# Kernel optimization log

Measured on AMD Instinct MI355X. Metric: run time of the kernel, lower is better.

The kernel has to match this reference:

```python
import jax, jax.numpy as jnp
import numpy as np

B, N, K = 4, 2048, 30
H = 128   # num_hidden == num_V_dim
E = 128   # num_E_dim
SCALE = 30.0
EPS = 1e-5


def _ln(x, g, b):
    m = jnp.mean(x, axis=-1, keepdims=True)
    v = jnp.mean(jnp.square(x - m), axis=-1, keepdims=True)
    return (x - m) * jax.lax.rsqrt(v + EPS) * g + b


def _gather_nodes(h_V, E_idx):
    # h_V: [B,N,D], E_idx: [B,N,K] -> [B,N,K,D]
    b, n, k = E_idx.shape
    flat = E_idx.reshape(b, n * k)
    g = jnp.take_along_axis(h_V, flat[:, :, None], axis=1)
    return g.reshape(b, n, k, h_V.shape[-1])


def _gelu(x):
    return jax.nn.gelu(x, approximate=False)  # torch GELU default (erf)


def _lin(x, w, b):
    return jnp.einsum('...i,oi->...o', x, w) + b


def setup_inputs() -> dict:
    key = jax.random.key(0)
    ks = jax.random.split(key, 24)
    s = 0.05
    inp = {
        'h_V': jax.random.normal(ks[0], (B, N, H), jnp.float32),
        'h_E': jax.random.normal(ks[1], (B, N, K, E), jnp.float32),
        'E_idx': jax.random.randint(ks[2], (B, N, K), 0, N, jnp.int32),
        'mask_V': jnp.ones((B, N), jnp.float32),
        'mask_attend': jnp.ones((B, N, K), jnp.float32),
        # node-update MLP W1,W2,W3
        'W1_w': jax.random.normal(ks[3], (H, E + 2 * H), jnp.float32) * s,
        'W1_b': jnp.zeros((H,), jnp.float32),
        'W2_w': jax.random.normal(ks[4], (H, H), jnp.float32) * s,
        'W2_b': jnp.zeros((H,), jnp.float32),
        'W3_w': jax.random.normal(ks[5], (H, H), jnp.float32) * s,
        'W3_b': jnp.zeros((H,), jnp.float32),
        # edge-update MLP W11,W12,W13
        'W11_w': jax.random.normal(ks[6], (H, E + 2 * H), jnp.float32) * s,
        'W11_b': jnp.zeros((H,), jnp.float32),
        'W12_w': jax.random.normal(ks[7], (H, H), jnp.float32) * s,
        'W12_b': jnp.zeros((H,), jnp.float32),
        'W13_w': jax.random.normal(ks[8], (E, H), jnp.float32) * s,
        'W13_b': jnp.zeros((E,), jnp.float32),
        # dense FFN
        'Win_w': jax.random.normal(ks[9], (4 * H, H), jnp.float32) * s,
        'Win_b': jnp.zeros((4 * H,), jnp.float32),
        'Wout_w': jax.random.normal(ks[10], (H, 4 * H), jnp.float32) * s,
        'Wout_b': jnp.zeros((H,), jnp.float32),
        # layer norms
        'g1': jnp.ones((H,), jnp.float32), 'b1': jnp.zeros((H,), jnp.float32),
        'g2': jnp.ones((H,), jnp.float32), 'b2': jnp.zeros((H,), jnp.float32),
        'g3': jnp.ones((E,), jnp.float32), 'b3': jnp.zeros((E,), jnp.float32),
    }
    return inp


def reference(h_V, h_E, E_idx, mask_V, mask_attend,
              W1_w, W1_b, W2_w, W2_b, W3_w, W3_b,
              W11_w, W11_b, W12_w, W12_b, W13_w, W13_b,
              Win_w, Win_b, Wout_w, Wout_b,
              g1, b1, g2, b2, g3, b3):
    # --- node update ---
    nb = _gather_nodes(h_V, E_idx)                               # [B,N,K,H]
    hV_exp = jnp.broadcast_to(h_V[:, :, None, :], nb.shape)
    h_EV = jnp.concatenate([hV_exp, h_E, nb], axis=-1)           # [B,N,K,E+2H]
    m = _lin(_gelu(_lin(_gelu(_lin(h_EV, W1_w, W1_b)), W2_w, W2_b)), W3_w, W3_b)
    m = mask_attend[..., None] * m
    dh = jnp.sum(m, axis=-2) / SCALE
    h_V = _ln(h_V + dh, g1, b1)
    dh = _lin(_gelu(_lin(h_V, Win_w, Win_b)), Wout_w, Wout_b)
    h_V = _ln(h_V + dh, g2, b2)
    h_V = mask_V[..., None] * h_V
    # --- edge update ---
    nb = _gather_nodes(h_V, E_idx)
    hV_exp = jnp.broadcast_to(h_V[:, :, None, :], nb.shape)
    h_EV = jnp.concatenate([hV_exp, h_E, nb], axis=-1)
    m = _lin(_gelu(_lin(_gelu(_lin(h_EV, W11_w, W11_b)), W12_w, W12_b)), W13_w, W13_b)
    h_E = _ln(h_E + m, g3, b3)
    return h_V, h_E
```

## Files before the change

kernel.cpp:

```cpp
#include <hip/hip_runtime.h>
#include <math.h>

#define Kn    30
#define Hn    128
#define NB    2048
#define YS    136

#define OFF_W1    0
#define OFF_W2    49152
#define OFF_W3    65536
#define OFF_W11   81920
#define OFF_W12   131072
#define OFF_W13   147456
#define OFF_WIN   163840
#define OFF_WOUT  229376
#define W_TOTAL   294912
#define WS_ZM     524288
#define WS_SS     1048576
#define WS_SN     2097152

typedef __attribute__((ext_vector_type(8)))  short bh8;
typedef __attribute__((ext_vector_type(4)))  short bh4;
typedef __attribute__((ext_vector_type(16))) float fx16;

__device__ __forceinline__ unsigned short f2bf(float f) {
    unsigned int u = __float_as_uint(f);
    u += 0x7fffu + ((u >> 16) & 1u);
    return (unsigned short)(u >> 16);
}
__device__ __forceinline__ float bf2f(unsigned short h) {
    return __uint_as_float(((unsigned int)h) << 16);
}
__device__ __forceinline__ float gelu_f(float x) {
    float u = 0.7978845608028654f * x * (1.0f + 0.044715f * x * x);
    return x / (1.0f + __expf(-2.0f * u));
}
__device__ __forceinline__ fx16 mfma_bf16(bh8 a, bh8 b, fx16 c) {
    return __builtin_amdgcn_mfma_f32_32x32x16_bf16(a, b, c, 0, 0, 0);
}
__device__ __forceinline__ void st_bf4(unsigned short* dst, float4 v) {
    bh4 t;
    t.x = (short)f2bf(v.x); t.y = (short)f2bf(v.y);
    t.z = (short)f2bf(v.z); t.w = (short)f2bf(v.w);
    *(bh4*)dst = t;
}

template<int KS>
__device__ __forceinline__ void gemm_one(const unsigned short* __restrict__ aBase,
                                         const unsigned short* __restrict__ b0,
                                         fx16& acc0) {
    #pragma unroll
    for (int ks = 0; ks < KS; ks++) {
        bh8 a = *(const bh8*)(aBase + ks * 16);
        acc0 = mfma_bf16(a, *(const bh8*)(b0 + ks * 16), acc0);
    }
}

__device__ __forceinline__ void epi_gelu_sg(const fx16& ac, int col, int rowBase,
                                            float bias, const float* __restrict__ sSelf,
                                            const float* __restrict__ nbrCol,
                                            const int* __restrict__ sIdx,
                                            unsigned short* __restrict__ dst, int lane) {
    int ro = rowBase + 4 * (lane >> 5);
    #pragma unroll
    for (int r = 0; r < 16; r++) {
        int row = ro + (r & 3) + 8 * (r >> 2);
        float st = sSelf[((row >= Kn) ? 128 : 0) + col];
        float pn = nbrCol[(size_t)sIdx[row] * Hn];
        dst[row * YS + col] = f2bf(gelu_f(ac[r] + bias + st + pn));
    }
}
__device__ __forceinline__ void epi_gelu(const fx16& ac, int col, int rowBase,
                                         float bias, unsigned short* __restrict__ dst,
                                         int lane) {
    int ro = rowBase + 4 * (lane >> 5);
    #pragma unroll
    for (int r = 0; r < 16; r++) {
        int row = ro + (r & 3) + 8 * (r >> 2);
        dst[row * YS + col] = f2bf(gelu_f(ac[r] + bias));
    }
}
__device__ __forceinline__ void epi_plain(const fx16& ac, int col, int rowBase,
                                          float bias, unsigned short* __restrict__ dst,
                                          int lane) {
    int ro = rowBase + 4 * (lane >> 5);
    #pragma unroll
    for (int r = 0; r < 16; r++) {
        int row = ro + (r & 3) + 8 * (r >> 2);
        dst[row * YS + col] = f2bf(ac[r] + bias);
    }
}

__global__ __launch_bounds__(256) void prep_weights(
    const float* __restrict__ W1, const float* __restrict__ W2,
    const float* __restrict__ W3, const float* __restrict__ W11,
    const float* __restrict__ W12, const float* __restrict__ W13,
    const float* __restrict__ Win, const float* __restrict__ Wout,
    unsigned short* __restrict__ wsbf) {
    int i = blockIdx.x * 256 + threadIdx.x;
    if (i >= W_TOTAL) return;
    float v;
    if      (i < OFF_W2)   v = W1[i - OFF_W1];
    else if (i < OFF_W3)   v = W2[i - OFF_W2];
    else if (i < OFF_W11)  v = W3[i - OFF_W3];
    else if (i < OFF_W12)  v = W11[i - OFF_W11];
    else if (i < OFF_W13)  v = W12[i - OFF_W12];
    else if (i < OFF_WIN)  v = W13[i - OFF_W13];
    else if (i < OFF_WOUT) v = Win[i - OFF_WIN];
    else                   v = Wout[i - OFF_WOUT];
    wsbf[i] = f2bf(v);
}

__global__ __launch_bounds__(256) void self_gemm(
    const float* __restrict__ hv, const unsigned short* __restrict__ wsbf,
    float* __restrict__ s1s, float* __restrict__ s1n) {
    __shared__ __align__(16) unsigned short sA[32 * YS];
    const int tid = threadIdx.x;
    const int p0 = blockIdx.x * 32;
    const unsigned short* W1bf = wsbf + OFF_W1;
    for (int i = tid; i < 1024; i += 256) {
        int r = i >> 5, c4 = (i & 31) << 2;
        float4 v = *(const float4*)(hv + (size_t)(p0 + r) * Hn + c4);
        st_bf4(sA + r * YS + c4, v);
    }
    __syncthreads();
    const int wid = tid >> 6, lane = tid & 63;
    const int lane31 = lane & 31, lk = (lane >> 5) << 3;
    fx16 accS = {}, accN = {};
    const unsigned short* a   = sA + lane31 * YS + lk;
    const unsigned short* bwS = W1bf + (size_t)(32 * wid + lane31) * 384 + lk;
    const unsigned short* bwN = bwS + 256;
    #pragma unroll
    for (int ks = 0; ks < 8; ks++) {
        bh8 av = *(const bh8*)(a + ks * 16);
        accS = mfma_bf16(av, *(const bh8*)(bwS + ks * 16), accS);
        accN = mfma_bf16(av, *(const bh8*)(bwN + ks * 16), accN);
    }
    int col = 32 * wid + lane31;
    #pragma unroll
    for (int r = 0; r < 16; r++) {
        int row = (r & 3) + 8 * (r >> 2) + 4 * (lane >> 5);
        s1s[(size_t)(p0 + row) * Hn + col] = accS[r];
        s1n[(size_t)(p0 + row) * Hn + col] = accN[r];
    }
}

__global__ __launch_bounds__(512, 8) void node_msg_mfma(
    const float* __restrict__ h_E, const int* __restrict__ E_idx,
    const float* __restrict__ mask_attend,
    const unsigned short* __restrict__ wsbf,
    const float* __restrict__ s1s, const float* __restrict__ s1n,
    const float* __restrict__ W1_b, const float* __restrict__ W2_b,
    unsigned short* __restrict__ zbf, float* __restrict__ zm) {
    __shared__ __align__(16) unsigned short sX[64 * YS];
    __shared__ __align__(16) unsigned short sY[64 * YS];
    __shared__ float sS1[256];
    __shared__ float sMask[64];
    __shared__ int   sIdx[64];

    const int tid = threadIdx.x;
    const int p0 = blockIdx.x * 2;
    const int bB = p0 >> 11;
    const unsigned short* W1bf = wsbf + OFF_W1;
    const unsigned short* W2bf = wsbf + OFF_W2;

    for (int i = tid; i < 1920; i += 512) {
        int r = i >> 5, c4 = (i & 31) << 2;
        float4 v = *(const float4*)(h_E + ((size_t)(p0 * Kn + r)) * Hn + c4);
        st_bf4(sX + r * YS + c4, v);
    }
    if (tid < 272)
        ((unsigned int*)(sX + 60 * YS))[tid] = 0;
    if (tid < 64) {
        int g = tid >> 5, c4 = (tid & 31) << 2;
        *(float4*)(sS1 + g * 128 + c4) = *(const float4*)(s1s + (size_t)(p0 + g) * Hn + c4);
    }
    if (tid < 60) sMask[tid] = mask_attend[p0 * Kn + tid];
    if (tid < 64) sIdx[tid] = (tid < 60) ? E_idx[p0 * Kn + tid] : 0;
    __syncthreads();

    const int wid = tid >> 6, lane = tid & 63;
    const int mt = wid & 1, ct = wid >> 1;
    const int lane31 = lane & 31, lk = (lane >> 5) << 3;
    const int rowBase = 32 * mt;
    const fx16 zv = {};
    const int col = 32 * ct + lane31;

    fx16 acc = zv;
    gemm_one<8>(sX + (rowBase + lane31) * YS + lk,
                W1bf + (size_t)col * 384 + 128 + lk, acc);
    epi_gelu_sg(acc, col, rowBase, W1_b[col], sS1,
                s1n + (size_t)bB * NB * Hn + col, sIdx, sY, lane);
    __syncthreads();

    acc = zv;
    gemm_one<8>(sY + (rowBase + lane31) * YS + lk,
                W2bf + (size_t)col * 128 + lk, acc);
    float* fbuf = (float*)sX;
    {
        float bias = W2_b[col];
        float sA0 = 0.f, sA1 = 0.f;
        #pragma unroll
        for (int r = 0; r < 16; r++) {
            int row = rowBase + (r & 3) + 8 * (r >> 2) + 4 * (lane >> 5);
            if (row < 60) {
                float v = gelu_f(acc[r] + bias) * sMask[row];
                if (row < Kn) sA0 += v; else sA1 += v;
            }
        }
        sA0 += __shfl_down(sA0, 32);
        sA1 += __shfl_down(sA1, 32);
        if (lane < 32) { fbuf[mt * 256 + col] = sA0; fbuf[mt * 256 + 128 + col] = sA1; }
    }
    __syncthreads();

    if (tid < 256) {
        int g = tid >> 7, c = tid & 127;
        float zval = (fbuf[g * 128 + c] + fbuf[256 + g * 128 + c]) * (1.0f / 30.0f);
        zbf[(size_t)(p0 + g) * Hn + c] = f2bf(zval);
    }
    if (tid < 2) {
        float s = 0.f;
        #pragma unroll
        for (int k = 0; k < 30; k++) s += sMask[tid * 30 + k];
        zm[p0 + tid] = s * (1.0f / 30.0f);
    }
}

__global__ __launch_bounds__(256) void node_fin_ffn(
    const unsigned short* __restrict__ zbf, const float* __restrict__ zm,
    const float* __restrict__ h_V, const float* __restrict__ mask_V,
    const unsigned short* __restrict__ wsbf,
    const float* __restrict__ W3_b, const float* __restrict__ Win_b,
    const float* __restrict__ Wout_b,
    const float* __restrict__ g1v, const float* __restrict__ b1v,
    const float* __restrict__ g2v, const float* __restrict__ b2v,
    float* __restrict__ hV_out, float* __restrict__ s11s, float* __restrict__ s11n) {
    __shared__ __align__(16) unsigned short sA[32 * YS];
    __shared__ __align__(16) unsigned short sH[32 * YS];
    __shared__ __align__(16) float sO[32 * 132];
    __shared__ __align__(16) float sM[32 * 132];
    __shared__ __align__(16) unsigned short sV[32 * YS];
    __shared__ float sZm[32];

    const int tid = threadIdx.x;
    const int p0 = blockIdx.x * 32;
    const unsigned short* W3bf   = wsbf + OFF_W3;
    const unsigned short* Winbf  = wsbf + OFF_WIN;
    const unsigned short* Woutbf = wsbf + OFF_WOUT;
    const unsigned short* W11bf  = wsbf + OFF_W11;

    for (int i = tid; i < 512; i += 256) {
        int r = i >> 4, c8 = (i & 15) << 3;
        *(bh8*)(sA + r * YS + c8) = *(const bh8*)(zbf + (size_t)(p0 + r) * Hn + c8);
    }
    if (tid < 32) sZm[tid] = zm[p0 + tid];
    __syncthreads();

    const int wid = tid >> 6, lane = tid & 63;
    const int lane31 = lane & 31, lk = (lane >> 5) << 3;
    const fx16 zv = {};

    {
        fx16 acc = zv;
        const unsigned short* a  = sA + lane31 * YS + lk;
        const unsigned short* bw = W3bf + (size_t)(32 * wid + lane31) * 128 + lk;
        #pragma unroll
        for (int ks = 0; ks < 8; ks++)
            acc = mfma_bf16(*(const bh8*)(a + ks * 16), *(const bh8*)(bw + ks * 16), acc);
        int col = 32 * wid + lane31;
        float bias = W3_b[col];
        #pragma unroll
        for (int r = 0; r < 16; r++) {
            int row = (r & 3) + 8 * (r >> 2) + 4 * (lane >> 5);
            sO[row * 132 + col] = acc[r] + sZm[row] * bias;
        }
    }
    __syncthreads();

    for (int r = wid; r < 32; r += 4) {
        float x0 = sO[r * 132 + lane]      + h_V[(size_t)(p0 + r) * Hn + lane];
        float x1 = sO[r * 132 + 64 + lane] + h_V[(size_t)(p0 + r) * Hn + 64 + lane];
        float s = x0 + x1, q = x0 * x0 + x1 * x1;
        #pragma unroll
        for (int off = 32; off; off >>= 1) { s += __shfl_down(s, off); q += __shfl_down(q, off); }
        s = __shfl(s, 0); q = __shfl(q, 0);
        float mean = s * 0.0078125f;
        float rstd = rsqrtf(q * 0.0078125f - mean * mean + 1e-5f);
        float m0 = (x0 - mean) * rstd * g1v[lane]      + b1v[lane];
        float m1 = (x1 - mean) * rstd * g1v[lane + 64] + b1v[lane + 64];
        sM[r * 132 + lane]      = m0;
        sM[r * 132 + 64 + lane] = m1;
        sA[r * YS + lane]      = f2bf(m0);
        sA[r * YS + 64 + lane] = f2bf(m1);
    }
    __syncthreads();

    fx16 accO = zv;
    for (int c = 0; c < 4; c++) {
        int hcol = 128 * c + 32 * wid + lane31;
        fx16 t = zv;
        {
            const unsigned short* a  = sA + lane31 * YS + lk;
            const unsigned short* bw = Winbf + (size_t)hcol * 128 + lk;
            #pragma unroll
            for (int ks = 0; ks < 8; ks++)
                t = mfma_bf16(*(const bh8*)(a + ks * 16), *(const bh8*)(bw + ks * 16), t);
        }
        float bias = Win_b[hcol];
        int colL = 32 * wid + lane31;
        #pragma unroll
        for (int r = 0; r < 16; r++) {
            int row = (r & 3) + 8 * (r >> 2) + 4 * (lane >> 5);
            sH[row * YS + colL] = f2bf(gelu_f(t[r] + bias));
        }
        __syncthreads();
        {
            const unsigned short* a  = sH + lane31 * YS + lk;
            const unsigned short* bw = Woutbf + (size_t)(32 * wid + lane31) * 512 + 128 * c + lk;
            #pragma unroll
            for (int ks = 0; ks < 8; ks++)
                accO = mfma_bf16(*(const bh8*)(a + ks * 16), *(const bh8*)(bw + ks * 16), accO);
        }
        __syncthreads();
    }
    {
        int col = 32 * wid + lane31;
        float bias = Wout_b[col];
        #pragma unroll
        for (int r = 0; r < 16; r++) {
            int row = (r & 3) + 8 * (r >> 2) + 4 * (lane >> 5);
            sO[row * 132 + col] = accO[r] + bias;
        }
    }
    __syncthreads();

    for (int r = wid; r < 32; r += 4) {
        float x0 = sO[r * 132 + lane]      + sM[r * 132 + lane];
        float x1 = sO[r * 132 + 64 + lane] + sM[r * 132 + 64 + lane];
        float s = x0 + x1, q = x0 * x0 + x1 * x1;
        #pragma unroll
        for (int off = 32; off; off >>= 1) { s += __shfl_down(s, off); q += __shfl_down(q, off); }
        s = __shfl(s, 0); q = __shfl(q, 0);
        float mean = s * 0.0078125f;
        float rstd = rsqrtf(q * 0.0078125f - mean * mean + 1e-5f);
        float mv = mask_V[p0 + r];
        float y0 = ((x0 - mean) * rstd * g2v[lane]      + b2v[lane])      * mv;
        float y1 = ((x1 - mean) * rstd * g2v[lane + 64] + b2v[lane + 64]) * mv;
        hV_out[(size_t)(p0 + r) * Hn + lane]      = y0;
        hV_out[(size_t)(p0 + r) * Hn + 64 + lane] = y1;
        sV[r * YS + lane]      = f2bf(y0);
        sV[r * YS + 64 + lane] = f2bf(y1);
    }
    __syncthreads();

    {
        int col = 32 * wid + lane31;
        fx16 accS = zv, accN = zv;
        const unsigned short* a   = sV + lane31 * YS + lk;
        const unsigned short* bwS = W11bf + (size_t)col * 384 + lk;
        const unsigned short* bwN = W11bf + (size_t)col * 384 + 256 + lk;
        #pragma unroll
        for (int ks = 0; ks < 8; ks++) {
            bh8 av = *(const bh8*)(a + ks * 16);
            accS = mfma_bf16(av, *(const bh8*)(bwS + ks * 16), accS);
            accN = mfma_bf16(av, *(const bh8*)(bwN + ks * 16), accN);
        }
        #pragma unroll
        for (int r = 0; r < 16; r++) {
            int row = (r & 3) + 8 * (r >> 2) + 4 * (lane >> 5);
            s11s[(size_t)(p0 + row) * Hn + col] = accS[r];
            s11n[(size_t)(p0 + row) * Hn + col] = accN[r];
        }
    }
}

__global__ __launch_bounds__(512, 8) void edge_update_mfma(
    const float* __restrict__ h_E, const int* __restrict__ E_idx,
    const unsigned short* __restrict__ wsbf,
    const float* __restrict__ s11s, const float* __restrict__ s11n,
    const float* __restrict__ W11_b, const float* __restrict__ W12_b,
    const float* __restrict__ W13_b,
    const float* __restrict__ g3v, const float* __restrict__ b3v,
    float* __restrict__ hE_out) {
    __shared__ __align__(16) unsigned short sX[64 * YS];
    __shared__ __align__(16) unsigned short sY[64 * YS];
    __shared__ float sS11[256];
    __shared__ int   sIdx[64];

    const int tid = threadIdx.x;
    const int p0 = blockIdx.x * 2;
    const int bB = p0 >> 11;
    const unsigned short* W11bf = wsbf + OFF_W11;
    const unsigned short* W12bf = wsbf + OFF_W12;
    const unsigned short* W13bf = wsbf + OFF_W13;

    for (int i = tid; i < 1920; i += 512) {
        int r = i >> 5, c4 = (i & 31) << 2;
        float4 v = *(const float4*)(h_E + ((size_t)(p0 * Kn + r)) * Hn + c4);
        st_bf4(sX + r * YS + c4, v);
    }
    if (tid < 272)
        ((unsigned int*)(sX + 60 * YS))[tid] = 0;
    if (tid < 64) {
        int g = tid >> 5, c4 = (tid & 31) << 2;
        *(float4*)(sS11 + g * 128 + c4) = *(const float4*)(s11s + (size_t)(p0 + g) * Hn + c4);
    }
    if (tid < 64) sIdx[tid] = (tid < 60) ? E_idx[p0 * Kn + tid] : 0;
    __syncthreads();

    const int wid = tid >> 6, lane = tid & 63;
    const int mt = wid & 1, ct = wid >> 1;
    const int lane31 = lane & 31, lk = (lane >> 5) << 3;
    const int rowBase = 32 * mt;
    const fx16 zv = {};
    const int col = 32 * ct + lane31;

    fx16 acc = zv;
    gemm_one<8>(sX + (rowBase + lane31) * YS + lk,
                W11bf + (size_t)col * 384 + 128 + lk, acc);
    epi_gelu_sg(acc, col, rowBase, W11_b[col], sS11,
                s11n + (size_t)bB * NB * Hn + col, sIdx, sY, lane);
    __syncthreads();

    acc = zv;
    gemm_one<8>(sY + (rowBase + lane31) * YS + lk,
                W12bf + (size_t)col * 128 + lk, acc);
    __syncthreads();
    epi_gelu(acc, col, rowBase, W12_b[col], sY, lane);
    __syncthreads();

    acc = zv;
    gemm_one<8>(sY + (rowBase + lane31) * YS + lk,
                W13bf + (size_t)col * 128 + lk, acc);
    __syncthreads();
    epi_plain(acc, col, rowBase, W13_b[col], sY, lane);
    __syncthreads();

    for (int r = wid; r < 60; r += 8) {
        float x0 = bf2f(sX[r * YS + lane])      + bf2f(sY[r * YS + lane]);
        float x1 = bf2f(sX[r * YS + 64 + lane]) + bf2f(sY[r * YS + 64 + lane]);
        float s = x0 + x1, q = x0 * x0 + x1 * x1;
        #pragma unroll
        for (int off = 32; off; off >>= 1) { s += __shfl_down(s, off); q += __shfl_down(q, off); }
        s = __shfl(s, 0); q = __shfl(q, 0);
        float mean = s * 0.0078125f;
        float rstd = rsqrtf(q * 0.0078125f - mean * mean + 1e-5f);
        float* op = hE_out + ((size_t)(p0 * Kn + r)) * 128;
        op[lane]      = (x0 - mean) * rstd * g3v[lane]      + b3v[lane];
        op[lane + 64] = (x1 - mean) * rstd * g3v[lane + 64] + b3v[lane + 64];
    }
}

extern "C" void kernel_launch(void* const* d_in, const int* in_sizes, int n_in,
                              void* d_out, int out_size, void* d_ws, size_t ws_size,
                              hipStream_t stream) {
    const float* h_V         = (const float*)d_in[0];
    const float* h_E         = (const float*)d_in[1];
    const int*   E_idx       = (const int*)  d_in[2];
    const float* mask_V      = (const float*)d_in[3];
    const float* mask_attend = (const float*)d_in[4];
    const float* W1_w  = (const float*)d_in[5];
    const float* W1_b  = (const float*)d_in[6];
    const float* W2_w  = (const float*)d_in[7];
    const float* W2_b  = (const float*)d_in[8];
    const float* W3_w  = (const float*)d_in[9];
    const float* W3_b  = (const float*)d_in[10];
    const float* W11_w = (const float*)d_in[11];
    const float* W11_b = (const float*)d_in[12];
    const float* W12_w = (const float*)d_in[13];
    const float* W12_b = (const float*)d_in[14];
    const float* W13_w = (const float*)d_in[15];
    const float* W13_b = (const float*)d_in[16];
    const float* Win_w  = (const float*)d_in[17];
    const float* Win_b  = (const float*)d_in[18];
    const float* Wout_w = (const float*)d_in[19];
    const float* Wout_b = (const float*)d_in[20];
    const float* g1 = (const float*)d_in[21];
    const float* b1 = (const float*)d_in[22];
    const float* g2 = (const float*)d_in[23];
    const float* b2 = (const float*)d_in[24];
    const float* g3 = (const float*)d_in[25];
    const float* b3 = (const float*)d_in[26];

    float* out    = (float*)d_out;
    float* hV_out = out;
    float* hE_out = out + (size_t)4 * 2048 * 128;
    unsigned short* wsbf = (unsigned short*)d_ws;
    float* wsf = (float*)(wsbf + W_TOTAL);
    unsigned short* zbf = (unsigned short*)wsf;
    float* zm = wsf + WS_ZM;
    float* sS = wsf + WS_SS;
    float* sN = wsf + WS_SN;

    prep_weights<<<(W_TOTAL + 255) / 256, 256, 0, stream>>>(
        W1_w, W2_w, W3_w, W11_w, W12_w, W13_w, Win_w, Wout_w, wsbf);

    self_gemm<<<256, 256, 0, stream>>>(h_V, wsbf, sS, sN);

    node_msg_mfma<<<4096, 512, 0, stream>>>(
        h_E, E_idx, mask_attend, wsbf, sS, sN, W1_b, W2_b, zbf, zm);

    node_fin_ffn<<<256, 256, 0, stream>>>(
        zbf, zm, h_V, mask_V, wsbf, W3_b, Win_b, Wout_b,
        g1, b1, g2, b2, hV_out, sS, sN);

    edge_update_mfma<<<4096, 512, 0, stream>>>(
        h_E, E_idx, wsbf, sS, sN,
        W11_b, W12_b, W13_b, g3, b3, hE_out);
}
```

Before: 482.3 us.

## Process one node per block and use a cheaper exp2/rcp GELU

The edge and node message kernels now handle one node (30 edge rows padded to 32) per 256-thread block instead of two nodes packed into 64 rows per 512-thread block. This shrinks the wasted padded MFMA rows from 4 of 64 to 2 of 32, drops the cross-wave shared-memory reduction in the node kernel, and halves LDS per block, which may allow more blocks per CU. The tanh-approx GELU is rewritten as a single exp2 and a hardware reciprocal with folded constants, which lowers epilogue ALU cost at a small accuracy cost. Twice as many blocks also means each block's weight loads are amortised over fewer rows.

```diff
diff --git a/kernel.cpp b/kernel.cpp
--- a/kernel.cpp
+++ b/kernel.cpp
@@ -32,8 +32,10 @@
     return __uint_as_float(((unsigned int)h) << 16);
 }
 __device__ __forceinline__ float gelu_f(float x) {
-    float u = 0.7978845608028654f * x * (1.0f + 0.044715f * x * x);
-    return x / (1.0f + __expf(-2.0f * u));
+    float x2 = x * x;
+    float p  = fmaf(x2, -0.10294415f, -2.30218409f);
+    float e  = exp2f(x * p);
+    return x * __builtin_amdgcn_rcpf(1.0f + e);
 }
 __device__ __forceinline__ fx16 mfma_bf16(bh8 a, bh8 b, fx16 c) {
     return __builtin_amdgcn_mfma_f32_32x32x16_bf16(a, b, c, 0, 0, 0);
@@ -56,34 +58,34 @@
     }
 }
 
-__device__ __forceinline__ void epi_gelu_sg(const fx16& ac, int col, int rowBase,
-                                            float bias, const float* __restrict__ sSelf,
-                                            const float* __restrict__ nbrCol,
-                                            const int* __restrict__ sIdx,
-                                            unsigned short* __restrict__ dst, int lane) {
-    int ro = rowBase + 4 * (lane >> 5);
+__device__ __forceinline__ void epi1_gelu_sg(const fx16& ac, int col,
+                                             float bias, const float* __restrict__ sSelf,
+                                             const float* __restrict__ nbrCol,
+                                             const int* __restrict__ sIdx,
+                                             unsigned short* __restrict__ dst, int lane) {
+    int ro = 4 * (lane >> 5);
+    float st = sSelf[col] + bias;
     #pragma unroll
     for (int r = 0; r < 16; r++) {
         int row = ro + (r & 3) + 8 * (r >> 2);
-        float st = sSelf[((row >= Kn) ? 128 : 0) + col];
         float pn = nbrCol[(size_t)sIdx[row] * Hn];
-        dst[row * YS + col] = f2bf(gelu_f(ac[r] + bias + st + pn));
-    }
-}
-__device__ __forceinline__ void epi_gelu(const fx16& ac, int col, int rowBase,
-                                         float bias, unsigned short* __restrict__ dst,
-                                         int lane) {
-    int ro = rowBase + 4 * (lane >> 5);
+        dst[row * YS + col] = f2bf(gelu_f(ac[r] + st + pn));
+    }
+}
+__device__ __forceinline__ void epi1_gelu(const fx16& ac, int col,
+                                          float bias, unsigned short* __restrict__ dst,
+                                          int lane) {
+    int ro = 4 * (lane >> 5);
     #pragma unroll
     for (int r = 0; r < 16; r++) {
         int row = ro + (r & 3) + 8 * (r >> 2);
         dst[row * YS + col] = f2bf(gelu_f(ac[r] + bias));
     }
 }
-__device__ __forceinline__ void epi_plain(const fx16& ac, int col, int rowBase,
-                                          float bias, unsigned short* __restrict__ dst,
-                                          int lane) {
-    int ro = rowBase + 4 * (lane >> 5);
+__device__ __forceinline__ void epi1_plain(const fx16& ac, int col,
+                                           float bias, unsigned short* __restrict__ dst,
+                                           int lane) {
+    int ro = 4 * (lane >> 5);
     #pragma unroll
     for (int r = 0; r < 16; r++) {
         int row = ro + (r & 3) + 8 * (r >> 2);
@@ -145,85 +147,74 @@
     }
 }
 
-__global__ __launch_bounds__(512, 8) void node_msg_mfma(
+__global__ __launch_bounds__(256, 8) void node_msg_mfma(
     const float* __restrict__ h_E, const int* __restrict__ E_idx,
     const float* __restrict__ mask_attend,
     const unsigned short* __restrict__ wsbf,
     const float* __restrict__ s1s, const float* __restrict__ s1n,
     const float* __restrict__ W1_b, const float* __restrict__ W2_b,
     unsigned short* __restrict__ zbf, float* __restrict__ zm) {
-    __shared__ __align__(16) unsigned short sX[64 * YS];
-    __shared__ __align__(16) unsigned short sY[64 * YS];
-    __shared__ float sS1[256];
-    __shared__ float sMask[64];
-    __shared__ int   sIdx[64];
+    __shared__ __align__(16) unsigned short sX[32 * YS];
+    __shared__ __align__(16) unsigned short sY[32 * YS];
+    __shared__ float sS1[128];
+    __shared__ float sMask[32];
+    __shared__ int   sIdx[32];
 
     const int tid = threadIdx.x;
-    const int p0 = blockIdx.x * 2;
-    const int bB = p0 >> 11;
+    const int p = blockIdx.x;
+    const int bB = p >> 11;
     const unsigned short* W1bf = wsbf + OFF_W1;
     const unsigned short* W2bf = wsbf + OFF_W2;
 
-    for (int i = tid; i < 1920; i += 512) {
+    for (int i = tid; i < 960; i += 256) {
         int r = i >> 5, c4 = (i & 31) << 2;
-        float4 v = *(const float4*)(h_E + ((size_t)(p0 * Kn + r)) * Hn + c4);
+        float4 v = *(const float4*)(h_E + ((size_t)p * Kn + r) * Hn + c4);
         st_bf4(sX + r * YS + c4, v);
     }
-    if (tid < 272)
-        ((unsigned int*)(sX + 60 * YS))[tid] = 0;
-    if (tid < 64) {
-        int g = tid >> 5, c4 = (tid & 31) << 2;
-        *(float4*)(sS1 + g * 128 + c4) = *(const float4*)(s1s + (size_t)(p0 + g) * Hn + c4);
-    }
-    if (tid < 60) sMask[tid] = mask_attend[p0 * Kn + tid];
-    if (tid < 64) sIdx[tid] = (tid < 60) ? E_idx[p0 * Kn + tid] : 0;
+    if (tid < 136)
+        ((unsigned int*)(sX + 30 * YS))[tid] = 0;
+    if (tid < 32) {
+        int c4 = tid << 2;
+        *(float4*)(sS1 + c4) = *(const float4*)(s1s + (size_t)p * Hn + c4);
+    }
+    if (tid < 32) {
+        sMask[tid] = (tid < Kn) ? mask_attend[p * Kn + tid] : 0.f;
+        sIdx[tid]  = (tid < Kn) ? E_idx[p * Kn + tid] : 0;
+    }
     __syncthreads();
 
     const int wid = tid >> 6, lane = tid & 63;
-    const int mt = wid & 1, ct = wid >> 1;
     const int lane31 = lane & 31, lk = (lane >> 5) << 3;
-    const int rowBase = 32 * mt;
     const fx16 zv = {};
-    const int col = 32 * ct + lane31;
+    const int col = 32 * wid + lane31;
 
     fx16 acc = zv;
-    gemm_one<8>(sX + (rowBase + lane31) * YS + lk,
+    gemm_one<8>(sX + lane31 * YS + lk,
                 W1bf + (size_t)col * 384 + 128 + lk, acc);
-    epi_gelu_sg(acc, col, rowBase, W1_b[col], sS1,
-                s1n + (size_t)bB * NB * Hn + col, sIdx, sY, lane);
+    epi1_gelu_sg(acc, col, W1_b[col], sS1,
+                 s1n + (size_t)bB * NB * Hn + col, sIdx, sY, lane);
     __syncthreads();
 
     acc = zv;
-    gemm_one<8>(sY + (rowBase + lane31) * YS + lk,
+    gemm_one<8>(sY + lane31 * YS + lk,
                 W2bf + (size_t)col * 128 + lk, acc);
-    float* fbuf = (float*)sX;
     {
         float bias = W2_b[col];
-        float sA0 = 0.f, sA1 = 0.f;
+        float sum = 0.f;
         #pragma unroll
         for (int r = 0; r < 16; r++) {
-            int row = rowBase + (r & 3) + 8 * (r >> 2) + 4 * (lane >> 5);
-            if (row < 60) {
-                float v = gelu_f(acc[r] + bias) * sMask[row];
-                if (row < Kn) sA0 += v; else sA1 += v;
-            }
-        }
-        sA0 += __shfl_down(sA0, 32);
-        sA1 += __shfl_down(sA1, 32);
-        if (lane < 32) { fbuf[mt * 256 + col] = sA0; fbuf[mt * 256 + 128 + col] = sA1; }
-    }
-    __syncthreads();
-
-    if (tid < 256) {
-        int g = tid >> 7, c = tid & 127;
-        float zval = (fbuf[g * 128 + c] + fbuf[256 + g * 128 + c]) * (1.0f / 30.0f);
-        zbf[(size_t)(p0 + g) * Hn + c] = f2bf(zval);
-    }
-    if (tid < 2) {
+            int row = (r & 3) + 8 * (r >> 2) + 4 * (lane >> 5);
+            if (row < Kn) sum += gelu_f(acc[r] + bias) * sMask[row];
+        }
+        sum += __shfl_down(sum, 32);
+        if (lane < 32)
+            zbf[(size_t)p * Hn + col] = f2bf(sum * (1.0f / 30.0f));
+    }
+    if (tid == 0) {
         float s = 0.f;
         #pragma unroll
-        for (int k = 0; k < 30; k++) s += sMask[tid * 30 + k];
-        zm[p0 + tid] = s * (1.0f / 30.0f);
+        for (int k = 0; k < Kn; k++) s += sMask[k];
+        zm[p] = s * (1.0f / 30.0f);
     }
 }
 
@@ -375,7 +366,7 @@
     }
 }
 
-__global__ __launch_bounds__(512, 8) void edge_update_mfma(
+__global__ __launch_bounds__(256, 8) void edge_update_mfma(
     const float* __restrict__ h_E, const int* __restrict__ E_idx,
     const unsigned short* __restrict__ wsbf,
     const float* __restrict__ s11s, const float* __restrict__ s11n,
@@ -383,61 +374,59 @@
     const float* __restrict__ W13_b,
     const float* __restrict__ g3v, const float* __restrict__ b3v,
     float* __restrict__ hE_out) {
-    __shared__ __align__(16) unsigned short sX[64 * YS];
-    __shared__ __align__(16) unsigned short sY[64 * YS];
-    __shared__ float sS11[256];
-    __shared__ int   sIdx[64];
+    __shared__ __align__(16) unsigned short sX[32 * YS];
+    __shared__ __align__(16) unsigned short sY[32 * YS];
+    __shared__ float sS11[128];
+    __shared__ int   sIdx[32];
 
     const int tid = threadIdx.x;
-    const int p0 = blockIdx.x * 2;
-    const int bB = p0 >> 11;
+    const int p = blockIdx.x;
+    const int bB = p >> 11;
     const unsigned short* W11bf = wsbf + OFF_W11;
     const unsigned short* W12bf = wsbf + OFF_W12;
     const unsigned short* W13bf = wsbf + OFF_W13;
 
-    for (int i = tid; i < 1920; i += 512) {
+    for (int i = tid; i < 960; i += 256) {
         int r = i >> 5, c4 = (i & 31) << 2;
-        float4 v = *(const float4*)(h_E + ((size_t)(p0 * Kn + r)) * Hn + c4);
+        float4 v = *(const float4*)(h_E + ((size_t)p * Kn + r) * Hn + c4);
         st_bf4(sX + r * YS + c4, v);
     }
-    if (tid < 272)
-        ((unsigned int*)(sX + 60 * YS))[tid] = 0;
-    if (tid < 64) {
-        int g = tid >> 5, c4 = (tid & 31) << 2;
-        *(float4*)(sS11 + g * 128 + c4) = *(const float4*)(s11s + (size_t)(p0 + g) * Hn + c4);
-    }
-    if (tid < 64) sIdx[tid] = (tid < 60) ? E_idx[p0 * Kn + tid] : 0;
+    if (tid < 136)
+        ((unsigned int*)(sX + 30 * YS))[tid] = 0;
+    if (tid < 32) {
+        int c4 = tid << 2;
+        *(float4*)(sS11 + c4) = *(const float4*)(s11s + (size_t)p * Hn + c4);
+    }
+    if (tid < 32) sIdx[tid] = (tid < Kn) ? E_idx[p * Kn + tid] : 0;
     __syncthreads();
 
     const int wid = tid >> 6, lane = tid & 63;
-    const int mt = wid & 1, ct = wid >> 1;
     const int lane31 = lane & 31, lk = (lane >> 5) << 3;
-    const int rowBase = 32 * mt;
     const fx16 zv = {};
-    const int col = 32 * ct + lane31;
+    const int col = 32 * wid + lane31;
 
     fx16 acc = zv;
-    gemm_one<8>(sX + (rowBase + lane31) * YS + lk,
+    gemm_one<8>(sX + lane31 * YS + lk,
                 W11bf + (size_t)col * 384 + 128 + lk, acc);
-    epi_gelu_sg(acc, col, rowBase, W11_b[col], sS11,
-                s11n + (size_t)bB * NB * Hn + col, sIdx, sY, lane);
+    epi1_gelu_sg(acc, col, W11_b[col], sS11,
+                 s11n + (size_t)bB * NB * Hn + col, sIdx, sY, lane);
     __syncthreads();
 
     acc = zv;
-    gemm_one<8>(sY + (rowBase + lane31) * YS + lk,
+    gemm_one<8>(sY + lane31 * YS + lk,
                 W12bf + (size_t)col * 128 + lk, acc);
     __syncthreads();
-    epi_gelu(acc, col, rowBase, W12_b[col], sY, lane);
+    epi1_gelu(acc, col, W12_b[col], sY, lane);
     __syncthreads();
 
     acc = zv;
-    gemm_one<8>(sY + (rowBase + lane31) * YS + lk,
+    gemm_one<8>(sY + lane31 * YS + lk,
                 W13bf + (size_t)col * 128 + lk, acc);
     __syncthreads();
-    epi_plain(acc, col, rowBase, W13_b[col], sY, lane);
-    __syncthreads();
-
-    for (int r = wid; r < 60; r += 8) {
+    epi1_plain(acc, col, W13_b[col], sY, lane);
+    __syncthreads();
+
+    for (int r = wid; r < Kn; r += 4) {
         float x0 = bf2f(sX[r * YS + lane])      + bf2f(sY[r * YS + lane]);
         float x1 = bf2f(sX[r * YS + 64 + lane]) + bf2f(sY[r * YS + 64 + lane]);
         float s = x0 + x1, q = x0 * x0 + x1 * x1;
@@ -446,7 +435,7 @@
         s = __shfl(s, 0); q = __shfl(q, 0);
         float mean = s * 0.0078125f;
         float rstd = rsqrtf(q * 0.0078125f - mean * mean + 1e-5f);
-        float* op = hE_out + ((size_t)(p0 * Kn + r)) * 128;
+        float* op = hE_out + ((size_t)p * Kn + r) * Hn;
         op[lane]      = (x0 - mean) * rstd * g3v[lane]      + b3v[lane];
         op[lane + 64] = (x1 - mean) * rstd * g3v[lane + 64] + b3v[lane + 64];
     }
@@ -498,14 +487,14 @@
 
     self_gemm<<<256, 256, 0, stream>>>(h_V, wsbf, sS, sN);
 
-    node_msg_mfma<<<4096, 512, 0, stream>>>(
+    node_msg_mfma<<<8192, 256, 0, stream>>>(
         h_E, E_idx, mask_attend, wsbf, sS, sN, W1_b, W2_b, zbf, zm);
 
     node_fin_ffn<<<256, 256, 0, stream>>>(
         zbf, zm, h_V, mask_V, wsbf, W3_b, Win_b, Wout_b,
         g1, b1, g2, b2, hV_out, sS, sN);
 
-    edge_update_mfma<<<4096, 512, 0, stream>>>(
+    edge_update_mfma<<<8192, 256, 0, stream>>>(
         h_E, E_idx, wsbf, sS, sN,
         W11_b, W12_b, W13_b, g3, b3, hE_out);
 }
```

Result: no change. 473.1 us (-1.9%).
